# Performance work log

Measured on AMD Instinct MI355X. Metric: run time of the kernel, lower is better.

The kernel has to match this reference:

```python
import jax, jax.numpy as jnp
import numpy as np

DIM_IN = 768
DIM_OUT = 64
SEQ = 4096
BATCH = 4

def setup_inputs() -> dict:
    key = jax.random.key(0)
    ks = jax.random.split(key, 7)
    s = 1.0 / np.sqrt(DIM_IN)
    return {
        "x": jax.random.normal(ks[0], (BATCH, SEQ, DIM_IN), dtype=jnp.float32),
        "wq": jax.random.uniform(ks[1], (DIM_IN, DIM_OUT), jnp.float32, -s, s),
        "bq": jax.random.uniform(ks[2], (DIM_OUT,), jnp.float32, -s, s),
        "wk": jax.random.uniform(ks[3], (DIM_IN, DIM_OUT), jnp.float32, -s, s),
        "bk": jax.random.uniform(ks[4], (DIM_OUT,), jnp.float32, -s, s),
        "wv": jax.random.uniform(ks[5], (DIM_IN, DIM_OUT), jnp.float32, -s, s),
        "bv": jax.random.uniform(ks[6], (DIM_OUT,), jnp.float32, -s, s),
    }

def reference(x, wq, bq, wk, bk, wv, bv):
    # QKV projections: (B, S, D_in) @ (D_in, D_out) + bias
    q = x @ wq + bq
    k = x @ wk + bk
    v = x @ wv + bv
    # full causal attention, scores scaled by sqrt(d_out) AFTER masking (as in source)
    scores = jnp.einsum('bqd,bkd->bqk', q, k)  # (B, S, S)
    seq = x.shape[1]
    causal = jnp.tril(jnp.ones((seq, seq), dtype=bool))  # True = keep
    scores = jnp.where(causal, scores, -jnp.inf)
    scale = 1.0 / np.sqrt(k.shape[-1]).astype(np.float32)
    weights = jax.nn.softmax(scores * scale, axis=-1)
    # dropout_rate = 0.0 -> identity
    return jnp.einsum('bqk,bkd->bqd', weights, v)
```

## Files before the change

kernel.cpp:

```cpp
#include <hip/hip_runtime.h>
#include <hip/hip_bf16.h>

#define BATCH 4
#define SEQ   4096
#define DIN   768
#define DOUT  64

typedef __attribute__((ext_vector_type(4))) float f32x4;
typedef __attribute__((ext_vector_type(8))) short short8;
typedef __attribute__((ext_vector_type(4))) short short4v;
typedef __attribute__((ext_vector_type(2))) unsigned uint2v;

#define QSCALE 0.18033688011112043f

static __device__ __forceinline__ unsigned short f2bf(float f) {
    union { float f; unsigned u; } un; un.f = f;
    unsigned r = un.u + 0x7FFF + ((un.u >> 16) & 1);
    return (unsigned short)(r >> 16);
}
static __device__ __forceinline__ float bf2f(unsigned short h) {
    union { unsigned u; float f; } un; un.u = ((unsigned)h) << 16;
    return un.f;
}
static __device__ __forceinline__ unsigned packbf(float lo, float hi) {
    return ((unsigned)f2bf(hi) << 16) | (unsigned)f2bf(lo);
}

__global__ void wprep_kernel(const float* __restrict__ wq,
                             const float* __restrict__ wk,
                             const float* __restrict__ wv,
                             unsigned short* __restrict__ wF) {
    __shared__ float lds[64][65];
    int o = blockIdx.x / 12, kt = blockIdx.x % 12;
    const float* w = (o == 0) ? wq : (o == 1) ? wk : wv;
    int tid = threadIdx.x;
    int k0 = kt * 64;
    #pragma unroll
    for (int i = 0; i < 16; ++i) {
        int flat = tid + i * 256;
        int kl = flat >> 6, n = flat & 63;
        lds[kl][n] = w[(k0 + kl) * 64 + n];
    }
    __syncthreads();
    int lane = tid & 63;
    int m = lane & 15, g = lane >> 4;
    #pragma unroll
    for (int i = 0; i < 2; ++i) {
        int f = i * 4 + (tid >> 6);
        int t = f >> 1, kcl = f & 1;
        int kc = kt * 2 + kcl;
        int nc = o * 4 + t;
        short8 v;
        #pragma unroll
        for (int j = 0; j < 8; ++j)
            v[j] = (short)f2bf(lds[kcl * 32 + g * 8 + j][t * 16 + m]);
        *(short8*)&wF[(size_t)(nc * 24 + kc) * 512 + lane * 8] = v;
    }
}

__global__ void __launch_bounds__(256) proj_kernel(
        const float* __restrict__ x,
        const float* __restrict__ bq,
        const float* __restrict__ bk,
        const float* __restrict__ bv,
        const unsigned short* __restrict__ wF,
        unsigned short* __restrict__ Qf,
        unsigned short* __restrict__ Kf,
        unsigned short* __restrict__ Vf) {
    __shared__ __align__(16) unsigned short xs[32][776];
    __shared__ unsigned short tr[4][16][24];

    int tid = threadIdx.x;
    int w = tid >> 6;
    int lane = tid & 63;
    int m = lane & 15, g = lane >> 4;
    int r0 = blockIdx.x * 32;

    {
        const float* xbase = x + (size_t)r0 * DIN;
        #pragma unroll
        for (int i = 0; i < 24; ++i) {
            int flat4 = tid + i * 256;
            int row = flat4 / 192;
            int c4 = flat4 - row * 192;
            float4 v = *(const float4*)(xbase + (size_t)row * DIN + c4 * 4);
            short4v sv;
            sv[0] = (short)f2bf(v.x); sv[1] = (short)f2bf(v.y);
            sv[2] = (short)f2bf(v.z); sv[3] = (short)f2bf(v.w);
            *(short4v*)&xs[row][c4 * 4] = sv;
        }
    }
    __syncthreads();

    f32x4 acc[2][3];
    #pragma unroll
    for (int st = 0; st < 2; ++st)
        #pragma unroll
        for (int t = 0; t < 3; ++t) acc[st][t] = (f32x4){0.f, 0.f, 0.f, 0.f};

    const unsigned short* wb0 = wF + (size_t)((w * 3 + 0) * 24) * 512 + lane * 8;
    const unsigned short* wb1 = wF + (size_t)((w * 3 + 1) * 24) * 512 + lane * 8;
    const unsigned short* wb2 = wF + (size_t)((w * 3 + 2) * 24) * 512 + lane * 8;

    short8 bf0 = *(const short8*)(wb0);
    short8 bf1 = *(const short8*)(wb1);
    short8 bf2 = *(const short8*)(wb2);
    short8 af0 = *(const short8*)&xs[m][g * 8];
    short8 af1 = *(const short8*)&xs[16 + m][g * 8];

    for (int kc = 0; kc < 24; ++kc) {
        short8 nb0, nb1, nb2, na0, na1;
        bool have = (kc + 1) < 24;
        if (have) {
            int off = (kc + 1) * 512;
            nb0 = *(const short8*)(wb0 + off);
            nb1 = *(const short8*)(wb1 + off);
            nb2 = *(const short8*)(wb2 + off);
            na0 = *(const short8*)&xs[m][(kc + 1) * 32 + g * 8];
            na1 = *(const short8*)&xs[16 + m][(kc + 1) * 32 + g * 8];
        }
        acc[0][0] = __builtin_amdgcn_mfma_f32_16x16x32_bf16(af0, bf0, acc[0][0], 0, 0, 0);
        acc[1][0] = __builtin_amdgcn_mfma_f32_16x16x32_bf16(af1, bf0, acc[1][0], 0, 0, 0);
        acc[0][1] = __builtin_amdgcn_mfma_f32_16x16x32_bf16(af0, bf1, acc[0][1], 0, 0, 0);
        acc[1][1] = __builtin_amdgcn_mfma_f32_16x16x32_bf16(af1, bf1, acc[1][1], 0, 0, 0);
        acc[0][2] = __builtin_amdgcn_mfma_f32_16x16x32_bf16(af0, bf2, acc[0][2], 0, 0, 0);
        acc[1][2] = __builtin_amdgcn_mfma_f32_16x16x32_bf16(af1, bf2, acc[1][2], 0, 0, 0);
        if (have) {
            bf0 = nb0; bf1 = nb1; bf2 = nb2;
            af0 = na0; af1 = na1;
        }
    }

    int b2 = r0 >> 12;
    int s = (r0 & 4095) >> 5;
    #pragma unroll
    for (int st = 0; st < 2; ++st) {
        #pragma unroll
        for (int tt = 0; tt < 3; ++tt) {
            int nc = w * 3 + tt;
            int o = nc >> 2;
            int t = nc & 3;
            const float* bias_p = (o == 0) ? bq : (o == 1) ? bk : bv;
            float bias = bias_p[t * 16 + m];
            #pragma unroll
            for (int r = 0; r < 4; ++r) {
                float val = acc[st][tt][r] + bias;
                if (o == 0) val *= QSCALE;
                tr[w][g * 4 + r][m] = f2bf(val);
            }
            if (o < 2) {
                if (g < 2) {
                    short8 v8;
                    #pragma unroll
                    for (int j = 0; j < 8; ++j) v8[j] = (short)tr[w][m][g * 8 + j];
                    unsigned short* dst = (o == 0) ? Qf : Kf;
                    int c = t >> 1;
                    *(short8*)&dst[(size_t)((blockIdx.x * 2 + st) * 2 + c) * 512
                                   + (((t & 1) * 2 + g) * 16 + m) * 8] = v8;
                }
            } else {
                if (g < 2) {
                    short8 v8;
                    #pragma unroll
                    for (int j = 0; j < 8; ++j) v8[j] = (short)tr[w][g * 8 + j][m];
                    *(short8*)&Vf[((size_t)(b2 * 128 + s) * 4 + t) * 512
                                  + ((st * 2 + g) * 16 + m) * 8] = v8;
                }
            }
        }
    }
}

__global__ void __launch_bounds__(512, 2) attn_kernel(
        const unsigned short* __restrict__ Qf,
        const unsigned short* __restrict__ Kf,
        const unsigned short* __restrict__ Vf,
        float* __restrict__ out) {
    __shared__ __align__(16) unsigned short PT[8][16][40];
    __shared__ __align__(16) unsigned short pacc[8][16][68];
    __shared__ float pm[8][16];
    __shared__ float pl[8][16];

    int j = blockIdx.x;
    int b = j & 3;
    int qt = j >> 2;
    int base0 = qt * 16;
    int base1 = (255 - qt) * 16;
    int ns0 = (qt + 2) >> 1;
    int ns1 = (257 - qt) >> 1;
    int tid = threadIdx.x;
    int w = tid >> 6;
    int lane = tid & 63;
    int m = lane & 15, g = lane >> 4;

    const unsigned short* Q0 = Qf + (size_t)(b * 256 + qt) * 1024 + lane * 8;
    const unsigned short* Q1 = Qf + (size_t)(b * 256 + 255 - qt) * 1024 + lane * 8;
    short8 qf00 = *(const short8*)(Q0);
    short8 qf01 = *(const short8*)(Q0 + 512);
    short8 qf10 = *(const short8*)(Q1);
    short8 qf11 = *(const short8*)(Q1 + 512);

    short8 onesA;
    #pragma unroll
    for (int jj = 0; jj < 8; ++jj) onesA[jj] = (short)0x3F80;

    f32x4 acc[2][5];
    #pragma unroll
    for (int rt = 0; rt < 2; ++rt)
        #pragma unroll
        for (int t = 0; t < 5; ++t) acc[rt][t] = (f32x4){0.f, 0.f, 0.f, 0.f};
    float mrun0 = -INFINITY, mrun1 = -INFINITY;

    const unsigned short* Kbase = Kf + (size_t)(b * 256) * 1024 + lane * 8;
    const unsigned short* Vbase = Vf + (size_t)(b * 128) * 2048 + lane * 8;

    short8 kf[4], vf[4];
    if (w < ns1) {
        #pragma unroll
        for (int t = 0; t < 4; ++t) {
            kf[t] = *(const short8*)(Kbase + (size_t)w * 2048 + t * 512);
            vf[t] = *(const short8*)(Vbase + (size_t)w * 2048 + t * 512);
        }
    }

    for (int s = w; s < ns1; s += 8) {
        int kv0 = s * 32;
        int sn = s + 8;
        bool have = (sn < ns1);
        bool do0 = (s < ns0);

        if (do0) {
            f32x4 st0 = (f32x4){0.f, 0.f, 0.f, 0.f};
            f32x4 st1 = (f32x4){0.f, 0.f, 0.f, 0.f};
            st0 = __builtin_amdgcn_mfma_f32_16x16x32_bf16(kf[0], qf00, st0, 0, 0, 0);
            st0 = __builtin_amdgcn_mfma_f32_16x16x32_bf16(kf[1], qf01, st0, 0, 0, 0);
            st1 = __builtin_amdgcn_mfma_f32_16x16x32_bf16(kf[2], qf00, st1, 0, 0, 0);
            st1 = __builtin_amdgcn_mfma_f32_16x16x32_bf16(kf[3], qf01, st1, 0, 0, 0);
            if (s == ns0 - 1) {
                int q = base0 + m;
                #pragma unroll
                for (int r = 0; r < 4; ++r) {
                    if (kv0 + g * 4 + r > q)      st0[r] = -INFINITY;
                    if (kv0 + 16 + g * 4 + r > q) st1[r] = -INFINITY;
                }
            }
            float th = mrun0 + 8.0f;
            bool need = (st0[0] > th) | (st0[1] > th) | (st0[2] > th) | (st0[3] > th)
                      | (st1[0] > th) | (st1[1] > th) | (st1[2] > th) | (st1[3] > th);
            if (__any(need)) {
                float rmax = fmaxf(fmaxf(fmaxf(st0[0], st0[1]), fmaxf(st0[2], st0[3])),
                                   fmaxf(fmaxf(st1[0], st1[1]), fmaxf(st1[2], st1[3])));
                rmax = fmaxf(rmax, __shfl_xor(rmax, 16));
                rmax = fmaxf(rmax, __shfl_xor(rmax, 32));
                float mnew = fmaxf(mrun0, rmax);
                float alpha = __builtin_amdgcn_exp2f(mrun0 - mnew);
                mrun0 = mnew;
                #pragma unroll
                for (int t = 0; t < 5; ++t)
                    #pragma unroll
                    for (int r = 0; r < 4; ++r) acc[0][t][r] *= alpha;
            }
            float p00 = __builtin_amdgcn_exp2f(st0[0] - mrun0);
            float p01 = __builtin_amdgcn_exp2f(st0[1] - mrun0);
            float p02 = __builtin_amdgcn_exp2f(st0[2] - mrun0);
            float p03 = __builtin_amdgcn_exp2f(st0[3] - mrun0);
            float p10 = __builtin_amdgcn_exp2f(st1[0] - mrun0);
            float p11 = __builtin_amdgcn_exp2f(st1[1] - mrun0);
            float p12 = __builtin_amdgcn_exp2f(st1[2] - mrun0);
            float p13 = __builtin_amdgcn_exp2f(st1[3] - mrun0);
            *(uint2v*)&PT[w][m][g * 4]      = (uint2v){packbf(p00, p01), packbf(p02, p03)};
            *(uint2v*)&PT[w][m][16 + g * 4] = (uint2v){packbf(p10, p11), packbf(p12, p13)};
            short8 pb = *(const short8*)&PT[w][m][g * 8];
            #pragma unroll
            for (int t = 0; t < 4; ++t)
                acc[0][t] = __builtin_amdgcn_mfma_f32_16x16x32_bf16(vf[t], pb, acc[0][t], 0, 0, 0);
            acc[0][4] = __builtin_amdgcn_mfma_f32_16x16x32_bf16(onesA, pb, acc[0][4], 0, 0, 0);
        }

        {
            f32x4 st0 = (f32x4){0.f, 0.f, 0.f, 0.f};
            f32x4 st1 = (f32x4){0.f, 0.f, 0.f, 0.f};
            st0 = __builtin_amdgcn_mfma_f32_16x16x32_bf16(kf[0], qf10, st0, 0, 0, 0);
            st0 = __builtin_amdgcn_mfma_f32_16x16x32_bf16(kf[1], qf11, st0, 0, 0, 0);
            st1 = __builtin_amdgcn_mfma_f32_16x16x32_bf16(kf[2], qf10, st1, 0, 0, 0);
            st1 = __builtin_amdgcn_mfma_f32_16x16x32_bf16(kf[3], qf11, st1, 0, 0, 0);

            if (have) {
                #pragma unroll
                for (int t = 0; t < 4; ++t)
                    kf[t] = *(const short8*)(Kbase + (size_t)sn * 2048 + t * 512);
            }

            if (s == ns1 - 1) {
                int q = base1 + m;
                #pragma unroll
                for (int r = 0; r < 4; ++r) {
                    if (kv0 + g * 4 + r > q)      st0[r] = -INFINITY;
                    if (kv0 + 16 + g * 4 + r > q) st1[r] = -INFINITY;
                }
            }
            float th = mrun1 + 8.0f;
            bool need = (st0[0] > th) | (st0[1] > th) | (st0[2] > th) | (st0[3] > th)
                      | (st1[0] > th) | (st1[1] > th) | (st1[2] > th) | (st1[3] > th);
            if (__any(need)) {
                float rmax = fmaxf(fmaxf(fmaxf(st0[0], st0[1]), fmaxf(st0[2], st0[3])),
                                   fmaxf(fmaxf(st1[0], st1[1]), fmaxf(st1[2], st1[3])));
                rmax = fmaxf(rmax, __shfl_xor(rmax, 16));
                rmax = fmaxf(rmax, __shfl_xor(rmax, 32));
                float mnew = fmaxf(mrun1, rmax);
                float alpha = __builtin_amdgcn_exp2f(mrun1 - mnew);
                mrun1 = mnew;
                #pragma unroll
                for (int t = 0; t < 5; ++t)
                    #pragma unroll
                    for (int r = 0; r < 4; ++r) acc[1][t][r] *= alpha;
            }
            float p00 = __builtin_amdgcn_exp2f(st0[0] - mrun1);
            float p01 = __builtin_amdgcn_exp2f(st0[1] - mrun1);
            float p02 = __builtin_amdgcn_exp2f(st0[2] - mrun1);
            float p03 = __builtin_amdgcn_exp2f(st0[3] - mrun1);
            float p10 = __builtin_amdgcn_exp2f(st1[0] - mrun1);
            float p11 = __builtin_amdgcn_exp2f(st1[1] - mrun1);
            float p12 = __builtin_amdgcn_exp2f(st1[2] - mrun1);
            float p13 = __builtin_amdgcn_exp2f(st1[3] - mrun1);
            *(uint2v*)&PT[w][m][g * 4]      = (uint2v){packbf(p00, p01), packbf(p02, p03)};
            *(uint2v*)&PT[w][m][16 + g * 4] = (uint2v){packbf(p10, p11), packbf(p12, p13)};
            short8 pb = *(const short8*)&PT[w][m][g * 8];
            #pragma unroll
            for (int t = 0; t < 4; ++t)
                acc[1][t] = __builtin_amdgcn_mfma_f32_16x16x32_bf16(vf[t], pb, acc[1][t], 0, 0, 0);
            acc[1][4] = __builtin_amdgcn_mfma_f32_16x16x32_bf16(onesA, pb, acc[1][4], 0, 0, 0);

            if (have) {
                #pragma unroll
                for (int t = 0; t < 4; ++t)
                    vf[t] = *(const short8*)(Vbase + (size_t)sn * 2048 + t * 512);
            }
        }
    }

    #pragma unroll
    for (int rt = 0; rt < 2; ++rt) {
        int qbase = (rt == 0) ? base0 : base1;
        float mr = (rt == 0) ? mrun0 : mrun1;
        if (lane < 16) {
            pm[w][m] = mr;
            pl[w][m] = acc[rt][4][0];
        }
        #pragma unroll
        for (int t = 0; t < 4; ++t)
            #pragma unroll
            for (int r = 0; r < 4; ++r)
                pacc[w][m][t * 16 + g * 4 + r] = f2bf(acc[rt][t][r]);
        __syncthreads();

        if (tid < 256) {
            int row = tid >> 4;
            int c4 = (tid & 15) * 4;
            float mmax = pm[0][row];
            #pragma unroll
            for (int w2 = 1; w2 < 8; ++w2) mmax = fmaxf(mmax, pm[w2][row]);
            float lt = 0.f;
            float o0 = 0.f, o1 = 0.f, o2 = 0.f, o3 = 0.f;
            #pragma unroll
            for (int w2 = 0; w2 < 8; ++w2) {
                float sc2 = __builtin_amdgcn_exp2f(pm[w2][row] - mmax);
                lt += pl[w2][row] * sc2;
                short4v pa4 = *(const short4v*)&pacc[w2][row][c4];
                o0 += bf2f((unsigned short)pa4[0]) * sc2;
                o1 += bf2f((unsigned short)pa4[1]) * sc2;
                o2 += bf2f((unsigned short)pa4[2]) * sc2;
                o3 += bf2f((unsigned short)pa4[3]) * sc2;
            }
            float invl = 1.0f / lt;
            float4 res = make_float4(o0 * invl, o1 * invl, o2 * invl, o3 * invl);
            *(float4*)&out[(size_t)(b * SEQ + qbase + row) * DOUT + c4] = res;
        }
        __syncthreads();
    }
}

extern "C" void kernel_launch(void* const* d_in, const int* in_sizes, int n_in,
                              void* d_out, int out_size, void* d_ws, size_t ws_size,
                              hipStream_t stream) {
    const float* x  = (const float*)d_in[0];
    const float* wq = (const float*)d_in[1];
    const float* bq = (const float*)d_in[2];
    const float* wk = (const float*)d_in[3];
    const float* bk = (const float*)d_in[4];
    const float* wv = (const float*)d_in[5];
    const float* bv = (const float*)d_in[6];
    float* out = (float*)d_out;

    char* ws = (char*)d_ws;
    unsigned short* wF = (unsigned short*)ws;
    unsigned short* Qf = (unsigned short*)(ws + 294912);
    unsigned short* Kf = (unsigned short*)(ws + 294912 + 2097152);
    unsigned short* Vf = (unsigned short*)(ws + 294912 + 4194304);

    wprep_kernel<<<36, 256, 0, stream>>>(wq, wk, wv, wF);
    proj_kernel<<<512, 256, 0, stream>>>(x, bq, bk, bv, wF, Qf, Kf, Vf);
    attn_kernel<<<512, 512, 0, stream>>>(Qf, Kf, Vf, out);
}
```

Before: 48.72 us.

## Process four query tiles per attention block to reuse K/V loads

Each attention block now handles four 16-row query tiles (qt, 127-qt, 128+qt, 255-qt) instead of two. Every K/V chunk loaded into registers is therefore reused across four score/PV computations, and the grid is halved to 256 blocks. Launch bounds drop to one block per CU to make room for the doubled accumulator registers. The cost is fewer blocks in flight and lower occupancy, which can expose more memory latency.

```diff
diff --git a/kernel.cpp b/kernel.cpp
--- a/kernel.cpp
+++ b/kernel.cpp
@@ -171,7 +171,7 @@
     }
 }
 
-__global__ void __launch_bounds__(512, 2) attn_kernel(
+__global__ void __launch_bounds__(512, 1) attn_kernel(
         const unsigned short* __restrict__ Qf,
         const unsigned short* __restrict__ Kf,
         const unsigned short* __restrict__ Vf,
@@ -184,38 +184,42 @@
     int j = blockIdx.x;
     int b = j & 3;
     int qt = j >> 2;
-    int base0 = qt * 16;
-    int base1 = (255 - qt) * 16;
-    int ns0 = (qt + 2) >> 1;
-    int ns1 = (257 - qt) >> 1;
+    int T[4];
+    T[0] = qt; T[1] = 127 - qt; T[2] = 128 + qt; T[3] = 255 - qt;
+    int ns[4], base[4];
+    #pragma unroll
+    for (int i = 0; i < 4; ++i) { base[i] = T[i] * 16; ns[i] = (T[i] + 2) >> 1; }
     int tid = threadIdx.x;
     int w = tid >> 6;
     int lane = tid & 63;
     int m = lane & 15, g = lane >> 4;
 
-    const unsigned short* Q0 = Qf + (size_t)(b * 256 + qt) * 1024 + lane * 8;
-    const unsigned short* Q1 = Qf + (size_t)(b * 256 + 255 - qt) * 1024 + lane * 8;
-    short8 qf00 = *(const short8*)(Q0);
-    short8 qf01 = *(const short8*)(Q0 + 512);
-    short8 qf10 = *(const short8*)(Q1);
-    short8 qf11 = *(const short8*)(Q1 + 512);
+    short8 qfr[4][2];
+    #pragma unroll
+    for (int i = 0; i < 4; ++i) {
+        const unsigned short* Qp = Qf + (size_t)(b * 256 + T[i]) * 1024 + lane * 8;
+        qfr[i][0] = *(const short8*)(Qp);
+        qfr[i][1] = *(const short8*)(Qp + 512);
+    }
 
     short8 onesA;
     #pragma unroll
     for (int jj = 0; jj < 8; ++jj) onesA[jj] = (short)0x3F80;
 
-    f32x4 acc[2][5];
-    #pragma unroll
-    for (int rt = 0; rt < 2; ++rt)
+    f32x4 acc[4][5];
+    #pragma unroll
+    for (int rt = 0; rt < 4; ++rt)
         #pragma unroll
         for (int t = 0; t < 5; ++t) acc[rt][t] = (f32x4){0.f, 0.f, 0.f, 0.f};
-    float mrun0 = -INFINITY, mrun1 = -INFINITY;
+    float mrun[4];
+    #pragma unroll
+    for (int rt = 0; rt < 4; ++rt) mrun[rt] = -INFINITY;
 
     const unsigned short* Kbase = Kf + (size_t)(b * 256) * 1024 + lane * 8;
     const unsigned short* Vbase = Vf + (size_t)(b * 128) * 2048 + lane * 8;
 
     short8 kf[4], vf[4];
-    if (w < ns1) {
+    if (w < ns[3]) {
         #pragma unroll
         for (int t = 0; t < 4; ++t) {
             kf[t] = *(const short8*)(Kbase + (size_t)w * 2048 + t * 512);
@@ -223,28 +227,38 @@
         }
     }
 
-    for (int s = w; s < ns1; s += 8) {
+    for (int s = w; s < ns[3]; s += 8) {
         int kv0 = s * 32;
         int sn = s + 8;
-        bool have = (sn < ns1);
-        bool do0 = (s < ns0);
-
-        if (do0) {
+        bool have = (sn < ns[3]);
+
+        #pragma unroll
+        for (int rt = 0; rt < 4; ++rt) {
+            if (rt < 3 && s >= ns[rt]) continue;
+
             f32x4 st0 = (f32x4){0.f, 0.f, 0.f, 0.f};
             f32x4 st1 = (f32x4){0.f, 0.f, 0.f, 0.f};
-            st0 = __builtin_amdgcn_mfma_f32_16x16x32_bf16(kf[0], qf00, st0, 0, 0, 0);
-            st0 = __builtin_amdgcn_mfma_f32_16x16x32_bf16(kf[1], qf01, st0, 0, 0, 0);
-            st1 = __builtin_amdgcn_mfma_f32_16x16x32_bf16(kf[2], qf00, st1, 0, 0, 0);
-            st1 = __builtin_amdgcn_mfma_f32_16x16x32_bf16(kf[3], qf01, st1, 0, 0, 0);
-            if (s == ns0 - 1) {
-                int q = base0 + m;
+            st0 = __builtin_amdgcn_mfma_f32_16x16x32_bf16(kf[0], qfr[rt][0], st0, 0, 0, 0);
+            st0 = __builtin_amdgcn_mfma_f32_16x16x32_bf16(kf[1], qfr[rt][1], st0, 0, 0, 0);
+            st1 = __builtin_amdgcn_mfma_f32_16x16x32_bf16(kf[2], qfr[rt][0], st1, 0, 0, 0);
+            st1 = __builtin_amdgcn_mfma_f32_16x16x32_bf16(kf[3], qfr[rt][1], st1, 0, 0, 0);
+
+            if (rt == 3 && have) {
+                #pragma unroll
+                for (int t = 0; t < 4; ++t)
+                    kf[t] = *(const short8*)(Kbase + (size_t)sn * 2048 + t * 512);
+            }
+
+            if (s == ns[rt] - 1) {
+                int q = base[rt] + m;
                 #pragma unroll
                 for (int r = 0; r < 4; ++r) {
                     if (kv0 + g * 4 + r > q)      st0[r] = -INFINITY;
                     if (kv0 + 16 + g * 4 + r > q) st1[r] = -INFINITY;
                 }
             }
-            float th = mrun0 + 8.0f;
+
+            float th = mrun[rt] + 8.0f;
             bool need = (st0[0] > th) | (st0[1] > th) | (st0[2] > th) | (st0[3] > th)
                       | (st1[0] > th) | (st1[1] > th) | (st1[2] > th) | (st1[3] > th);
             if (__any(need)) {
@@ -252,99 +266,42 @@
                                    fmaxf(fmaxf(st1[0], st1[1]), fmaxf(st1[2], st1[3])));
                 rmax = fmaxf(rmax, __shfl_xor(rmax, 16));
                 rmax = fmaxf(rmax, __shfl_xor(rmax, 32));
-                float mnew = fmaxf(mrun0, rmax);
-                float alpha = __builtin_amdgcn_exp2f(mrun0 - mnew);
-                mrun0 = mnew;
+                float mnew = fmaxf(mrun[rt], rmax);
+                float alpha = __builtin_amdgcn_exp2f(mrun[rt] - mnew);
+                mrun[rt] = mnew;
                 #pragma unroll
                 for (int t = 0; t < 5; ++t)
                     #pragma unroll
-                    for (int r = 0; r < 4; ++r) acc[0][t][r] *= alpha;
-            }
-            float p00 = __builtin_amdgcn_exp2f(st0[0] - mrun0);
-            float p01 = __builtin_amdgcn_exp2f(st0[1] - mrun0);
-            float p02 = __builtin_amdgcn_exp2f(st0[2] - mrun0);
-            float p03 = __builtin_amdgcn_exp2f(st0[3] - mrun0);
-            float p10 = __builtin_amdgcn_exp2f(st1[0] - mrun0);
-            float p11 = __builtin_amdgcn_exp2f(st1[1] - mrun0);
-            float p12 = __builtin_amdgcn_exp2f(st1[2] - mrun0);
-            float p13 = __builtin_amdgcn_exp2f(st1[3] - mrun0);
+                    for (int r = 0; r < 4; ++r) acc[rt][t][r] *= alpha;
+            }
+            float p00 = __builtin_amdgcn_exp2f(st0[0] - mrun[rt]);
+            float p01 = __builtin_amdgcn_exp2f(st0[1] - mrun[rt]);
+            float p02 = __builtin_amdgcn_exp2f(st0[2] - mrun[rt]);
+            float p03 = __builtin_amdgcn_exp2f(st0[3] - mrun[rt]);
+            float p10 = __builtin_amdgcn_exp2f(st1[0] - mrun[rt]);
+            float p11 = __builtin_amdgcn_exp2f(st1[1] - mrun[rt]);
+            float p12 = __builtin_amdgcn_exp2f(st1[2] - mrun[rt]);
+            float p13 = __builtin_amdgcn_exp2f(st1[3] - mrun[rt]);
             *(uint2v*)&PT[w][m][g * 4]      = (uint2v){packbf(p00, p01), packbf(p02, p03)};
             *(uint2v*)&PT[w][m][16 + g * 4] = (uint2v){packbf(p10, p11), packbf(p12, p13)};
             short8 pb = *(const short8*)&PT[w][m][g * 8];
             #pragma unroll
             for (int t = 0; t < 4; ++t)
-                acc[0][t] = __builtin_amdgcn_mfma_f32_16x16x32_bf16(vf[t], pb, acc[0][t], 0, 0, 0);
-            acc[0][4] = __builtin_amdgcn_mfma_f32_16x16x32_bf16(onesA, pb, acc[0][4], 0, 0, 0);
-        }
-
-        {
-            f32x4 st0 = (f32x4){0.f, 0.f, 0.f, 0.f};
-            f32x4 st1 = (f32x4){0.f, 0.f, 0.f, 0.f};
-            st0 = __builtin_amdgcn_mfma_f32_16x16x32_bf16(kf[0], qf10, st0, 0, 0, 0);
-            st0 = __builtin_amdgcn_mfma_f32_16x16x32_bf16(kf[1], qf11, st0, 0, 0, 0);
-            st1 = __builtin_amdgcn_mfma_f32_16x16x32_bf16(kf[2], qf10, st1, 0, 0, 0);
-            st1 = __builtin_amdgcn_mfma_f32_16x16x32_bf16(kf[3], qf11, st1, 0, 0, 0);
-
-            if (have) {
-                #pragma unroll
-                for (int t = 0; t < 4; ++t)
-                    kf[t] = *(const short8*)(Kbase + (size_t)sn * 2048 + t * 512);
-            }
-
-            if (s == ns1 - 1) {
-                int q = base1 + m;
-                #pragma unroll
-                for (int r = 0; r < 4; ++r) {
-                    if (kv0 + g * 4 + r > q)      st0[r] = -INFINITY;
-                    if (kv0 + 16 + g * 4 + r > q) st1[r] = -INFINITY;
-                }
-            }
-            float th = mrun1 + 8.0f;
-            bool need = (st0[0] > th) | (st0[1] > th) | (st0[2] > th) | (st0[3] > th)
-                      | (st1[0] > th) | (st1[1] > th) | (st1[2] > th) | (st1[3] > th);
-            if (__any(need)) {
-                float rmax = fmaxf(fmaxf(fmaxf(st0[0], st0[1]), fmaxf(st0[2], st0[3])),
-                                   fmaxf(fmaxf(st1[0], st1[1]), fmaxf(st1[2], st1[3])));
-                rmax = fmaxf(rmax, __shfl_xor(rmax, 16));
-                rmax = fmaxf(rmax, __shfl_xor(rmax, 32));
-                float mnew = fmaxf(mrun1, rmax);
-                float alpha = __builtin_amdgcn_exp2f(mrun1 - mnew);
-                mrun1 = mnew;
-                #pragma unroll
-                for (int t = 0; t < 5; ++t)
-                    #pragma unroll
-                    for (int r = 0; r < 4; ++r) acc[1][t][r] *= alpha;
-            }
-            float p00 = __builtin_amdgcn_exp2f(st0[0] - mrun1);
-            float p01 = __builtin_amdgcn_exp2f(st0[1] - mrun1);
-            float p02 = __builtin_amdgcn_exp2f(st0[2] - mrun1);
-            float p03 = __builtin_amdgcn_exp2f(st0[3] - mrun1);
-            float p10 = __builtin_amdgcn_exp2f(st1[0] - mrun1);
-            float p11 = __builtin_amdgcn_exp2f(st1[1] - mrun1);
-            float p12 = __builtin_amdgcn_exp2f(st1[2] - mrun1);
-            float p13 = __builtin_amdgcn_exp2f(st1[3] - mrun1);
-            *(uint2v*)&PT[w][m][g * 4]      = (uint2v){packbf(p00, p01), packbf(p02, p03)};
-            *(uint2v*)&PT[w][m][16 + g * 4] = (uint2v){packbf(p10, p11), packbf(p12, p13)};
-            short8 pb = *(const short8*)&PT[w][m][g * 8];
+                acc[rt][t] = __builtin_amdgcn_mfma_f32_16x16x32_bf16(vf[t], pb, acc[rt][t], 0, 0, 0);
+            acc[rt][4] = __builtin_amdgcn_mfma_f32_16x16x32_bf16(onesA, pb, acc[rt][4], 0, 0, 0);
+        }
+
+        if (have) {
             #pragma unroll
             for (int t = 0; t < 4; ++t)
-                acc[1][t] = __builtin_amdgcn_mfma_f32_16x16x32_bf16(vf[t], pb, acc[1][t], 0, 0, 0);
-            acc[1][4] = __builtin_amdgcn_mfma_f32_16x16x32_bf16(onesA, pb, acc[1][4], 0, 0, 0);
-
-            if (have) {
-                #pragma unroll
-                for (int t = 0; t < 4; ++t)
-                    vf[t] = *(const short8*)(Vbase + (size_t)sn * 2048 + t * 512);
-            }
-        }
-    }
-
-    #pragma unroll
-    for (int rt = 0; rt < 2; ++rt) {
-        int qbase = (rt == 0) ? base0 : base1;
-        float mr = (rt == 0) ? mrun0 : mrun1;
+                vf[t] = *(const short8*)(Vbase + (size_t)sn * 2048 + t * 512);
+        }
+    }
+
+    #pragma unroll
+    for (int rt = 0; rt < 4; ++rt) {
         if (lane < 16) {
-            pm[w][m] = mr;
+            pm[w][m] = mrun[rt];
             pl[w][m] = acc[rt][4][0];
         }
         #pragma unroll
@@ -374,7 +331,7 @@
             }
             float invl = 1.0f / lt;
             float4 res = make_float4(o0 * invl, o1 * invl, o2 * invl, o3 * invl);
-            *(float4*)&out[(size_t)(b * SEQ + qbase + row) * DOUT + c4] = res;
+            *(float4*)&out[(size_t)(b * SEQ + base[rt] + row) * DOUT + c4] = res;
         }
         __syncthreads();
     }
@@ -400,5 +357,5 @@
 
     wprep_kernel<<<36, 256, 0, stream>>>(wq, wk, wv, wF);
     proj_kernel<<<512, 256, 0, stream>>>(x, bq, bk, bv, wF, Qf, Kf, Vf);
-    attn_kernel<<<512, 512, 0, stream>>>(Qf, Kf, Vf, out);
-}
+    attn_kernel<<<256, 512, 0, stream>>>(Qf, Kf, Vf, out);
+}
```

Measured after the change: 49.19 us. About the same (+1.0%).
